# Kernel optimization log

Hardware: AMD Instinct MI355X
Metric: run time of the kernel (lower is better)

## Reference

```python
import jax, jax.numpy as jnp
import numpy as np

N = 100000   # nodes
E = 1600000  # edges
B = 64       # graphs
F = 16       # node features
H = 128      # hidden dim
G = 8        # graph features
C = 2        # classes
NGIN = 2     # extra GIN layers after the first
BN_EPS = 1e-5


def elu01(x):
    # F.elu with alpha=0.1
    return jnp.where(x > 0, x, 0.1 * jnp.expm1(x))


def batchnorm(h, gamma, beta):
    # training-mode BatchNorm1d: biased batch statistics
    mu = h.mean(axis=0)
    var = h.var(axis=0)
    return (h - mu) * jax.lax.rsqrt(var + BN_EPS) * gamma + beta


def gin_layer(x, src, dst, W1, b1, gm, bt, W2, b2):
    # GINConv eps=0: MLP(x + sum_{j->i} x_j), then ELU(0.1)
    agg = jax.ops.segment_sum(x[src], dst, num_segments=x.shape[0])
    h = (x + agg) @ W1 + b1
    h = jax.nn.relu(batchnorm(h, gm, bt))
    return elu01(h @ W2 + b2)


def setup_inputs() -> dict:
    key = jax.random.key(0)
    ks = jax.random.split(key, 24)
    s = 0.05
    inp = {
        "h0": jax.random.normal(ks[0], (N, F), jnp.float32),
        "coord0": jax.random.normal(ks[1], (N, 3), jnp.float32),
        "g0": jax.random.normal(ks[2], (B, G), jnp.float32),
        "edge_index": jax.random.randint(ks[3], (2, E), 0, N, jnp.int32),
        "batch": jnp.sort(jax.random.randint(ks[4], (N,), 0, B, jnp.int32)),
        # first GIN layer: (F+3) -> H -> H
        "w1_0": jax.random.normal(ks[5], (F + 3, H), jnp.float32) * s,
        "b1_0": jnp.zeros((H,), jnp.float32),
        "gm_0": jnp.ones((H,), jnp.float32),
        "bt_0": jnp.zeros((H,), jnp.float32),
        "w2_0": jax.random.normal(ks[6], (H, H), jnp.float32) * s,
        "b2_0": jnp.zeros((H,), jnp.float32),
        # NGIN stacked layers: H -> H -> H
        "w1_r": jax.random.normal(ks[7], (NGIN, H, H), jnp.float32) * s,
        "b1_r": jnp.zeros((NGIN, H), jnp.float32),
        "gm_r": jnp.ones((NGIN, H), jnp.float32),
        "bt_r": jnp.zeros((NGIN, H), jnp.float32),
        "w2_r": jax.random.normal(ks[8], (NGIN, H, H), jnp.float32) * s,
        "b2_r": jnp.zeros((NGIN, H), jnp.float32),
        # classifier: (2H+G) -> H -> C
        "cw1": jax.random.normal(ks[9], (2 * H + G, H), jnp.float32) * s,
        "cb1": jnp.zeros((H,), jnp.float32),
        "cgm": jnp.ones((H,), jnp.float32),
        "cbt": jnp.zeros((H,), jnp.float32),
        "cw2": jax.random.normal(ks[10], (H, C), jnp.float32) * s,
        "cb2": jnp.zeros((C,), jnp.float32),
    }
    return inp


def reference(h0, coord0, g0, edge_index, batch,
              w1_0, b1_0, gm_0, bt_0, w2_0, b2_0,
              w1_r, b1_r, gm_r, bt_r, w2_r, b2_r,
              cw1, cb1, cgm, cbt, cw2, cb2):
    src, dst = edge_index[0], edge_index[1]
    x = jnp.concatenate([h0, coord0], axis=1)  # [N, F+3]
    x = gin_layer(x, src, dst, w1_0, b1_0, gm_0, bt_0, w2_0, b2_0)
    for i in range(NGIN):
        x = gin_layer(x, src, dst, w1_r[i], b1_r[i], gm_r[i], bt_r[i], w2_r[i], b2_r[i])
    # global mean + max pooling per graph
    nb = g0.shape[0]
    cnt = jax.ops.segment_sum(jnp.ones((x.shape[0], 1), x.dtype), batch, num_segments=nb)
    mean_p = jax.ops.segment_sum(x, batch, num_segments=nb) / jnp.maximum(cnt, 1.0)
    max_p = jax.ops.segment_max(x, batch, num_segments=nb)
    pooled = jnp.concatenate([mean_p, max_p], axis=-1)  # [B, 2H]
    z = jnp.concatenate([pooled, g0], axis=1)           # [B, 2H+G]
    z = elu01(z @ cw1 + cb1)
    z = batchnorm(z, cgm, cbt)
    logits = z @ cw2 + cb2
    return jax.nn.softmax(logits, axis=1)
```

## Files before the change

### kernel.cpp

```cpp
#include <hip/hip_runtime.h>
#include <math.h>

#define NN 100000
#define EE 1600000
#define BB 64
#define FF 16
#define HH 128
#define GG 8
#define K0 19
#define BN_EPS 1e-5f
#define PCH 16
#define BSHIFT 8
#define BNODES 256
#define NBINS 391
#define BCAP 8192
#define ACH 2048

typedef short bf16x8 __attribute__((ext_vector_type(8)));
typedef float f32x4 __attribute__((ext_vector_type(4)));

__device__ __forceinline__ float elu01f(float v) {
    return v > 0.f ? v : 0.1f * (__expf(v) - 1.f);
}

__device__ __forceinline__ unsigned f2bfu(float f) {
    unsigned u = __float_as_uint(f);
    unsigned r = u + 0x7FFFu + ((u >> 16) & 1u);
    return r >> 16;
}
__device__ __forceinline__ short f2bf(float f) { return (short)f2bfu(f); }
__device__ __forceinline__ float bfu2f(unsigned short b) {
    return __uint_as_float(((unsigned)b) << 16);
}
__device__ __forceinline__ float bflo(unsigned u) { return __uint_as_float(u << 16); }
__device__ __forceinline__ float bfhi(unsigned u) { return __uint_as_float(u & 0xffff0000u); }

__global__ __launch_bounds__(256) void k_binA(const int* __restrict__ esrc, const int* __restrict__ edst,
                                              int* __restrict__ bincnt, uint2* __restrict__ binbuf) {
    __shared__ int hist[NBINS];
    __shared__ int gbase[NBINS];
    __shared__ int cur[NBINS];
    __shared__ int sc[512];
    __shared__ uint2 ebuf[ACH];
    __shared__ uint2 sorted[ACH];
    int tid = threadIdx.x;
    int e0 = blockIdx.x * ACH;
    int n = min(ACH, EE - e0);
    for (int i = tid; i < NBINS; i += 256) hist[i] = 0;
    __syncthreads();
    for (int i = tid; i < n; i += 256) {
        int s = esrc[e0 + i];
        int d = edst[e0 + i];
        ebuf[i] = make_uint2((unsigned)s, (unsigned)d);
        atomicAdd(&hist[d >> BSHIFT], 1);
    }
    __syncthreads();
    sc[tid] = (tid < NBINS) ? hist[tid] : 0;
    sc[tid + 256] = (tid + 256 < NBINS) ? hist[tid + 256] : 0;
    __syncthreads();
    for (int off = 1; off < 512; off <<= 1) {
        int a0 = sc[tid], a1 = sc[tid + 256];
        int b0 = (tid >= off) ? sc[tid - off] : 0;
        int b1 = (tid + 256 >= off) ? sc[tid + 256 - off] : 0;
        __syncthreads();
        sc[tid] = a0 + b0;
        sc[tid + 256] = a1 + b1;
        __syncthreads();
    }
    for (int b = tid; b < NBINS; b += 256) {
        int c = hist[b];
        gbase[b] = (c > 0) ? atomicAdd(&bincnt[b], c) : 0;
        cur[b] = (b > 0) ? sc[b - 1] : 0;
    }
    __syncthreads();
    for (int i = tid; i < n; i += 256) {
        uint2 e = ebuf[i];
        int b = (int)(e.y >> BSHIFT);
        int pos = atomicAdd(&cur[b], 1);
        sorted[pos] = e;
    }
    __syncthreads();
    for (int i = tid; i < n; i += 256) {
        uint2 e = sorted[i];
        int b = (int)(e.y >> BSHIFT);
        int ls = (b > 0) ? sc[b - 1] : 0;
        int gpos = gbase[b] + (i - ls);
        binbuf[(size_t)b * BCAP + gpos] = e;
    }
}

__global__ void k_binscan(const int* __restrict__ bincnt, int* __restrict__ binstart, int* __restrict__ rp,
                          const int* __restrict__ batch, int* __restrict__ gptr) {
    __shared__ int sc[512];
    int t = threadIdx.x;
    sc[t] = (t < NBINS) ? bincnt[t] : 0;
    __syncthreads();
    for (int off = 1; off < 512; off <<= 1) {
        int v = (t >= off) ? sc[t - off] : 0;
        __syncthreads();
        sc[t] += v;
        __syncthreads();
    }
    if (t < NBINS) binstart[t] = (t > 0) ? sc[t - 1] : 0;
    if (t == 0) rp[NN] = EE;
    if (t <= BB) {
        int lo = 0, hi = NN;
        while (lo < hi) { int mid = (lo + hi) >> 1; if (batch[mid] < t) lo = mid + 1; else hi = mid; }
        gptr[t] = lo;
    }
}

__global__ __launch_bounds__(256) void k_binB(const uint2* __restrict__ binbuf, const int* __restrict__ bincnt,
                                              const int* __restrict__ binstart,
                                              int* __restrict__ rp, int* __restrict__ srcs) {
    __shared__ int hist[BNODES];
    __shared__ int scx[BNODES];
    __shared__ int scur[BNODES];
    __shared__ int sbuf[BCAP];
    int b = blockIdx.x;
    int n = bincnt[b];
    int tid = threadIdx.x;
    hist[tid] = 0;
    __syncthreads();
    const uint2* eb = binbuf + (size_t)b * BCAP;
    for (int i = tid; i < n; i += 256)
        atomicAdd(&hist[eb[i].y & (BNODES - 1)], 1);
    __syncthreads();
    scx[tid] = hist[tid];
    __syncthreads();
    for (int off = 1; off < 256; off <<= 1) {
        int v = (tid >= off) ? scx[tid - off] : 0;
        __syncthreads();
        scx[tid] += v;
        __syncthreads();
    }
    int base = binstart[b];
    int excl = (tid > 0) ? scx[tid - 1] : 0;
    int node = (b << BSHIFT) + tid;
    if (node < NN) rp[node] = base + excl;
    scur[tid] = excl;
    __syncthreads();
    for (int i = tid; i < n; i += 256) {
        uint2 e = eb[i];
        int pos = atomicAdd(&scur[e.y & (BNODES - 1)], 1);
        sbuf[pos] = (int)e.x;
    }
    __syncthreads();
    for (int i = tid; i < n; i += 256) srcs[base + i] = sbuf[i];
}

__global__ __launch_bounds__(256) void k_wprep(const float* __restrict__ w2_0, const float* __restrict__ w1_r,
                                               const float* __restrict__ w2_r, short* __restrict__ wt) {
    int t = blockIdx.x * 256 + threadIdx.x;
    if (t >= 5 * HH * HH) return;
    int m = t >> 14;
    int rem = t & 16383;
    int col = rem >> 7;
    int k = rem & 127;
    const float* src = (m == 0) ? w2_0 : (m <= 2 ? w1_r + (size_t)(m - 1) * HH * HH
                                                 : w2_r + (size_t)(m - 3) * HH * HH);
    wt[t] = f2bf(src[k * HH + col]);
}

__global__ __launch_bounds__(256) void k_buildx0(const float* __restrict__ h0, const float* __restrict__ coord,
                                                 unsigned short* __restrict__ x0) {
    int i = blockIdx.x * 256 + threadIdx.x;
    if (i >= NN * 32) return;
    int node = i >> 5, k = i & 31;
    float v = 0.f;
    if (k < FF) v = h0[node * FF + k];
    else if (k < K0) v = coord[node * 3 + (k - FF)];
    x0[i] = (unsigned short)f2bfu(v);
}

__global__ __launch_bounds__(256) void k_agg_small(const uint4* __restrict__ x, const int* __restrict__ rp,
                                                   const int* __restrict__ srcs, uint4* __restrict__ y) {
    int w = (blockIdx.x * 256 + threadIdx.x) >> 6;
    int lane = threadIdx.x & 63;
    if (w >= NN) return;
    int e = lane >> 2, q = lane & 3;
    int beg = rp[w], end = rp[w + 1];
    float acc[8];
    {
        if (e == 0) {
            uint4 u = x[(size_t)w * 4 + q];
            acc[0] = bflo(u.x); acc[1] = bfhi(u.x);
            acc[2] = bflo(u.y); acc[3] = bfhi(u.y);
            acc[4] = bflo(u.z); acc[5] = bfhi(u.z);
            acc[6] = bflo(u.w); acc[7] = bfhi(u.w);
        } else {
            #pragma unroll
            for (int j = 0; j < 8; j++) acc[j] = 0.f;
        }
    }
    for (int p = beg; p < end; p += 16) {
        int rem = end - p;
        bool act = e < rem;
        int sn = act ? srcs[p + e] : 0;
        uint4 u = x[(size_t)sn * 4 + q];
        float m = act ? 1.f : 0.f;
        acc[0] = fmaf(m, bflo(u.x), acc[0]); acc[1] = fmaf(m, bfhi(u.x), acc[1]);
        acc[2] = fmaf(m, bflo(u.y), acc[2]); acc[3] = fmaf(m, bfhi(u.y), acc[3]);
        acc[4] = fmaf(m, bflo(u.z), acc[4]); acc[5] = fmaf(m, bfhi(u.z), acc[5]);
        acc[6] = fmaf(m, bflo(u.w), acc[6]); acc[7] = fmaf(m, bfhi(u.w), acc[7]);
    }
    #pragma unroll
    for (int mask = 4; mask <= 32; mask <<= 1)
        #pragma unroll
        for (int j = 0; j < 8; j++)
            acc[j] += __shfl_xor(acc[j], mask, 64);
    if (e == 0) {
        uint4 o;
        o.x = f2bfu(acc[0]) | (f2bfu(acc[1]) << 16);
        o.y = f2bfu(acc[2]) | (f2bfu(acc[3]) << 16);
        o.z = f2bfu(acc[4]) | (f2bfu(acc[5]) << 16);
        o.w = f2bfu(acc[6]) | (f2bfu(acc[7]) << 16);
        y[(size_t)w * 4 + q] = o;
    }
}

__global__ __launch_bounds__(256) void k_agg128_bf(const unsigned* __restrict__ x, const int* __restrict__ rp,
                                                   const int* __restrict__ srcs, unsigned* __restrict__ y) {
    int w = (blockIdx.x * 256 + threadIdx.x) >> 6;
    int lane = threadIdx.x & 63;
    if (w >= NN) return;
    int beg = rp[w], end = rp[w + 1];
    unsigned us = x[(size_t)w * 64 + lane];
    float ax = bflo(us), ay = bfhi(us);
    float bx = 0.f, by = 0.f;
    float cx = 0.f, cy = 0.f;
    float dx = 0.f, dy = 0.f;
    int p = beg;
    for (; p + 16 <= end; p += 16) {
        int s0 = srcs[p + 0], s1 = srcs[p + 1], s2 = srcs[p + 2], s3 = srcs[p + 3];
        int s4 = srcs[p + 4], s5 = srcs[p + 5], s6 = srcs[p + 6], s7 = srcs[p + 7];
        int s8 = srcs[p + 8], s9 = srcs[p + 9], sa = srcs[p + 10], sb = srcs[p + 11];
        int sc_ = srcs[p + 12], sd = srcs[p + 13], se = srcs[p + 14], sf = srcs[p + 15];
        unsigned u0 = x[(size_t)s0 * 64 + lane];
        unsigned u1 = x[(size_t)s1 * 64 + lane];
        unsigned u2 = x[(size_t)s2 * 64 + lane];
        unsigned u3 = x[(size_t)s3 * 64 + lane];
        unsigned u4 = x[(size_t)s4 * 64 + lane];
        unsigned u5 = x[(size_t)s5 * 64 + lane];
        unsigned u6 = x[(size_t)s6 * 64 + lane];
        unsigned u7 = x[(size_t)s7 * 64 + lane];
        unsigned u8 = x[(size_t)s8 * 64 + lane];
        unsigned u9 = x[(size_t)s9 * 64 + lane];
        unsigned ua = x[(size_t)sa * 64 + lane];
        unsigned ub = x[(size_t)sb * 64 + lane];
        unsigned uc = x[(size_t)sc_ * 64 + lane];
        unsigned ud = x[(size_t)sd * 64 + lane];
        unsigned ue = x[(size_t)se * 64 + lane];
        unsigned uf = x[(size_t)sf * 64 + lane];
        ax += (bflo(u0) + bflo(u1)) + (bflo(u2) + bflo(u3));
        ay += (bfhi(u0) + bfhi(u1)) + (bfhi(u2) + bfhi(u3));
        bx += (bflo(u4) + bflo(u5)) + (bflo(u6) + bflo(u7));
        by += (bfhi(u4) + bfhi(u5)) + (bfhi(u6) + bfhi(u7));
        cx += (bflo(u8) + bflo(u9)) + (bflo(ua) + bflo(ub));
        cy += (bfhi(u8) + bfhi(u9)) + (bfhi(ua) + bfhi(ub));
        dx += (bflo(uc) + bflo(ud)) + (bflo(ue) + bflo(uf));
        dy += (bfhi(uc) + bfhi(ud)) + (bfhi(ue) + bfhi(uf));
    }
    for (; p + 8 <= end; p += 8) {
        int s0 = srcs[p + 0], s1 = srcs[p + 1], s2 = srcs[p + 2], s3 = srcs[p + 3];
        int s4 = srcs[p + 4], s5 = srcs[p + 5], s6 = srcs[p + 6], s7 = srcs[p + 7];
        unsigned u0 = x[(size_t)s0 * 64 + lane];
        unsigned u1 = x[(size_t)s1 * 64 + lane];
        unsigned u2 = x[(size_t)s2 * 64 + lane];
        unsigned u3 = x[(size_t)s3 * 64 + lane];
        unsigned u4 = x[(size_t)s4 * 64 + lane];
        unsigned u5 = x[(size_t)s5 * 64 + lane];
        unsigned u6 = x[(size_t)s6 * 64 + lane];
        unsigned u7 = x[(size_t)s7 * 64 + lane];
        ax += (bflo(u0) + bflo(u1)) + (bflo(u2) + bflo(u3));
        ay += (bfhi(u0) + bfhi(u1)) + (bfhi(u2) + bfhi(u3));
        bx += (bflo(u4) + bflo(u5)) + (bflo(u6) + bflo(u7));
        by += (bfhi(u4) + bfhi(u5)) + (bfhi(u6) + bfhi(u7));
    }
    for (; p < end; ++p) {
        unsigned u = x[(size_t)srcs[p] * 64 + lane];
        ax += bflo(u);
        ay += bfhi(u);
    }
    ax += bx + cx + dx;
    ay += by + cy + dy;
    y[(size_t)w * 64 + lane] = f2bfu(ax) | (f2bfu(ay) << 16);
}

template<int K, bool STATS>
__global__ __launch_bounds__(256) void k_gemm_small(const unsigned short* __restrict__ in,
        const float* __restrict__ W, const float* __restrict__ bias,
        unsigned short* __restrict__ out, float* __restrict__ part) {
    constexpr int SK = ((K + 3) / 4) * 4 + 4;
    __shared__ __align__(16) float yt[32 * SK];
    __shared__ float red[256];
    int tid = threadIdx.x;
    int row0 = blockIdx.x * 32;
    for (int t = tid; t < 32 * SK; t += 256) {
        int r = t / SK, k = t - r * SK;
        float v = 0.f;
        if (k < K) v = bfu2f(in[(size_t)(row0 + r) * 32 + k]);
        yt[t] = v;
    }
    __syncthreads();
    int col = tid & 127;
    int rg = tid >> 7;
    float acc[16];
    #pragma unroll
    for (int r = 0; r < 16; r++) acc[r] = 0.f;
    const float* ybase = &yt[rg * 16 * SK];
    int kk = 0;
    for (; kk + 4 <= K; kk += 4) {
        float w0 = W[(kk + 0) * HH + col];
        float w1 = W[(kk + 1) * HH + col];
        float w2 = W[(kk + 2) * HH + col];
        float w3 = W[(kk + 3) * HH + col];
        #pragma unroll
        for (int r = 0; r < 16; r++) {
            const float4 v = *(const float4*)&ybase[r * SK + kk];
            acc[r] = fmaf(v.x, w0, acc[r]);
            acc[r] = fmaf(v.y, w1, acc[r]);
            acc[r] = fmaf(v.z, w2, acc[r]);
            acc[r] = fmaf(v.w, w3, acc[r]);
        }
    }
    if constexpr (K % 4 != 0) {
        float w[4];
        #pragma unroll
        for (int j = 0; j < 4; j++) w[j] = (kk + j < K) ? W[(kk + j) * HH + col] : 0.f;
        #pragma unroll
        for (int r = 0; r < 16; r++) {
            const float4 v = *(const float4*)&ybase[r * SK + kk];
            acc[r] = fmaf(v.x, w[0], acc[r]);
            acc[r] = fmaf(v.y, w[1], acc[r]);
            acc[r] = fmaf(v.z, w[2], acc[r]);
            acc[r] = fmaf(v.w, w[3], acc[r]);
        }
    }
    float bcol = bias[col];
    float s = 0.f, s2 = 0.f;
    #pragma unroll
    for (int r = 0; r < 16; r++) {
        float hv = acc[r] + bcol;
        out[(size_t)(row0 + rg * 16 + r) * HH + col] = (unsigned short)f2bfu(hv);
        if (STATS) { s += hv; s2 = fmaf(hv, hv, s2); }
    }
    if (STATS) {
        red[tid] = s; __syncthreads();
        if (tid < 128) part[(size_t)blockIdx.x * 256 + tid] = s + red[tid + 128];
        __syncthreads();
        red[tid] = s2; __syncthreads();
        if (tid < 128) part[(size_t)blockIdx.x * 256 + 128 + tid] = s2 + red[tid + 128];
    }
}

template<bool STATS, bool BNIN, bool ELUOUT>
__global__ __launch_bounds__(256) void k_gemm_mfma(const unsigned short* __restrict__ in,
        const short* __restrict__ WT, const float* __restrict__ bias,
        const float* __restrict__ bnscale, const float* __restrict__ bnshift,
        unsigned short* __restrict__ out, float* __restrict__ part) {
    __shared__ __align__(16) short Al[64 * 136];
    __shared__ float lsum[HH], lsq[HH];
    int tid = threadIdx.x;
    int row0 = blockIdx.x * 64;
    if (STATS && tid < HH) { lsum[tid] = 0.f; lsq[tid] = 0.f; }
    {
        int r = tid >> 2;
        int k0 = (tid & 3) * 32;
        int grow = row0 + r;
        short* dst = &Al[r * 136 + k0];
        if (grow < NN) {
            const uint4* s4 = (const uint4*)(in + (size_t)grow * HH + k0);
            if constexpr (!BNIN) {
                uint4* d4 = (uint4*)dst;
                d4[0] = s4[0]; d4[1] = s4[1]; d4[2] = s4[2]; d4[3] = s4[3];
            } else {
                unsigned* d = (unsigned*)dst;
                #pragma unroll
                for (int q = 0; q < 4; q++) {
                    uint4 u = s4[q];
                    float4 sc0 = *(const float4*)(bnscale + k0 + q * 8);
                    float4 sh0 = *(const float4*)(bnshift + k0 + q * 8);
                    float4 sc1 = *(const float4*)(bnscale + k0 + q * 8 + 4);
                    float4 sh1 = *(const float4*)(bnshift + k0 + q * 8 + 4);
                    float a0 = bflo(u.x), a1 = bfhi(u.x);
                    float a2 = bflo(u.y), a3 = bfhi(u.y);
                    float a4 = bflo(u.z), a5 = bfhi(u.z);
                    float a6 = bflo(u.w), a7 = bfhi(u.w);
                    a0 = fmaxf(fmaf(a0, sc0.x, sh0.x), 0.f);
                    a1 = fmaxf(fmaf(a1, sc0.y, sh0.y), 0.f);
                    a2 = fmaxf(fmaf(a2, sc0.z, sh0.z), 0.f);
                    a3 = fmaxf(fmaf(a3, sc0.w, sh0.w), 0.f);
                    a4 = fmaxf(fmaf(a4, sc1.x, sh1.x), 0.f);
                    a5 = fmaxf(fmaf(a5, sc1.y, sh1.y), 0.f);
                    a6 = fmaxf(fmaf(a6, sc1.z, sh1.z), 0.f);
                    a7 = fmaxf(fmaf(a7, sc1.w, sh1.w), 0.f);
                    d[q * 4 + 0] = f2bfu(a0) | (f2bfu(a1) << 16);
                    d[q * 4 + 1] = f2bfu(a2) | (f2bfu(a3) << 16);
                    d[q * 4 + 2] = f2bfu(a4) | (f2bfu(a5) << 16);
                    d[q * 4 + 3] = f2bfu(a6) | (f2bfu(a7) << 16);
                }
            }
        } else {
            uint4 z = {0, 0, 0, 0};
            uint4* d4 = (uint4*)dst;
            d4[0] = z; d4[1] = z; d4[2] = z; d4[3] = z;
        }
    }
    __syncthreads();
    int wave = tid >> 6;
    int lane = tid & 63;
    int ln = lane & 15, quad = lane >> 4;
    int wcol0 = wave * 32;
    f32x4 acc[4][2];
    #pragma unroll
    for (int rt = 0; rt < 4; rt++)
        #pragma unroll
        for (int ct = 0; ct < 2; ct++) acc[rt][ct] = (f32x4){0.f, 0.f, 0.f, 0.f};
    #pragma unroll
    for (int ks = 0; ks < 4; ks++) {
        bf16x8 a[4], b[2];
        #pragma unroll
        for (int ct = 0; ct < 2; ct++)
            b[ct] = *(const bf16x8*)(WT + (size_t)(wcol0 + ct * 16 + ln) * HH + ks * 32 + quad * 8);
        #pragma unroll
        for (int rt = 0; rt < 4; rt++)
            a[rt] = *(const bf16x8*)(&Al[(rt * 16 + ln) * 136 + ks * 32 + quad * 8]);
        #pragma unroll
        for (int rt = 0; rt < 4; rt++)
            #pragma unroll
            for (int ct = 0; ct < 2; ct++)
                acc[rt][ct] = __builtin_amdgcn_mfma_f32_16x16x32_bf16(a[rt], b[ct], acc[rt][ct], 0, 0, 0);
    }
    float b0 = bias[wcol0 + ln];
    float b1 = bias[wcol0 + 16 + ln];
    float s[2] = {0.f, 0.f}, s2[2] = {0.f, 0.f};
    #pragma unroll
    for (int rt = 0; rt < 4; rt++) {
        #pragma unroll
        for (int r = 0; r < 4; r++) {
            int grow = row0 + rt * 16 + quad * 4 + r;
            if (grow < NN) {
                float hv0 = acc[rt][0][r] + b0;
                float hv1 = acc[rt][1][r] + b1;
                if (ELUOUT) { hv0 = elu01f(hv0); hv1 = elu01f(hv1); }
                out[(size_t)grow * HH + wcol0 + ln] = (unsigned short)f2bfu(hv0);
                out[(size_t)grow * HH + wcol0 + 16 + ln] = (unsigned short)f2bfu(hv1);
                if (STATS) {
                    s[0] += hv0; s2[0] = fmaf(hv0, hv0, s2[0]);
                    s[1] += hv1; s2[1] = fmaf(hv1, hv1, s2[1]);
                }
            }
        }
    }
    if (STATS) {
        atomicAdd(&lsum[wcol0 + ln], s[0]);
        atomicAdd(&lsum[wcol0 + 16 + ln], s[1]);
        atomicAdd(&lsq[wcol0 + ln], s2[0]);
        atomicAdd(&lsq[wcol0 + 16 + ln], s2[1]);
        __syncthreads();
        if (tid < HH) {
            part[(size_t)blockIdx.x * 256 + tid] = lsum[tid];
            part[(size_t)blockIdx.x * 256 + 128 + tid] = lsq[tid];
        }
    }
}

__global__ __launch_bounds__(256) void k_statred(const float* __restrict__ part, float* __restrict__ part2,
                                                 int nrows) {
    int tid = threadIdx.x;
    float acc = 0.f;
    for (int r = blockIdx.x; r < nrows; r += 64)
        acc += part[(size_t)r * 256 + tid];
    part2[(size_t)blockIdx.x * 256 + tid] = acc;
}

__global__ void k_bnfin(const float* __restrict__ part2, const float* __restrict__ gm,
                        const float* __restrict__ bt, float* scale, float* shift) {
    int c = threadIdx.x;
    float s = 0.f, s2 = 0.f;
    #pragma unroll 4
    for (int j = 0; j < 64; ++j) {
        s += part2[(size_t)j * 256 + c];
        s2 += part2[(size_t)j * 256 + 128 + c];
    }
    float mu = s * (1.f / NN);
    float var = fmaxf(s2 * (1.f / NN) - mu * mu, 0.f);
    float a = gm[c] * rsqrtf(var + BN_EPS);
    scale[c] = a;
    shift[c] = fmaf(-mu, a, bt[c]);
}

__global__ __launch_bounds__(128) void k_pool_part(const unsigned short* __restrict__ x,
                                                   const int* __restrict__ gptr,
                                                   float* __restrict__ psum, float* __restrict__ pmax) {
    int g = blockIdx.x >> 4;
    int ch = blockIdx.x & 15;
    int s = gptr[g], e = gptr[g + 1];
    int len = e - s;
    int per = (len + PCH - 1) / PCH;
    int lo = s + ch * per;
    int hi = min(lo + per, e);
    int c = threadIdx.x;
    float sm = 0.f, mx = -INFINITY;
    for (int i = lo; i < hi; ++i) {
        float v = bfu2f(x[(size_t)i * HH + c]);
        sm += v; mx = fmaxf(mx, v);
    }
    psum[(size_t)blockIdx.x * HH + c] = sm;
    pmax[(size_t)blockIdx.x * HH + c] = mx;
}

__global__ __launch_bounds__(128) void k_pool_cls1(const float* __restrict__ psum, const float* __restrict__ pmax,
                                                   const int* __restrict__ gptr, const float* __restrict__ g0,
                                                   const float* __restrict__ cw1, const float* __restrict__ cb1,
                                                   float* __restrict__ z1) {
    __shared__ float zr[264];
    int g = blockIdx.x, c = threadIdx.x;
    float sm = 0.f, mx = -INFINITY;
    for (int ch = 0; ch < PCH; ++ch) {
        sm += psum[(size_t)(g * PCH + ch) * HH + c];
        mx = fmaxf(mx, pmax[(size_t)(g * PCH + ch) * HH + c]);
    }
    int cntn = gptr[g + 1] - gptr[g];
    zr[c] = sm / (float)max(cntn, 1);
    zr[128 + c] = mx;
    if (c < GG) zr[256 + c] = g0[g * GG + c];
    __syncthreads();
    float acc = cb1[c];
    for (int k = 0; k < 264; ++k) acc = fmaf(zr[k], cw1[k * HH + c], acc);
    z1[g * HH + c] = elu01f(acc);
}

__global__ __launch_bounds__(128) void k_cls2(const float* __restrict__ z1, const float* __restrict__ cgm,
                                              const float* __restrict__ cbt, const float* __restrict__ cw2,
                                              const float* __restrict__ cb2, float* __restrict__ outp) {
    __shared__ float zn[HH * 65];
    int c = threadIdx.x;
    float s = 0.f, s2 = 0.f;
    for (int g = 0; g < BB; ++g) {
        float v = z1[g * HH + c];
        s += v; s2 = fmaf(v, v, s2);
    }
    float mu = s * (1.f / BB);
    float var = fmaxf(s2 * (1.f / BB) - mu * mu, 0.f);
    float a = cgm[c] * rsqrtf(var + BN_EPS);
    float sh = fmaf(-mu, a, cbt[c]);
    for (int g = 0; g < BB; ++g) zn[c * 65 + g] = fmaf(z1[g * HH + c], a, sh);
    __syncthreads();
    if (c < BB) {
        float l0 = cb2[0], l1 = cb2[1];
        for (int k = 0; k < HH; ++k) {
            float v = zn[k * 65 + c];
            l0 = fmaf(v, cw2[k * 2 + 0], l0);
            l1 = fmaf(v, cw2[k * 2 + 1], l1);
        }
        float m = fmaxf(l0, l1);
        float e0 = __expf(l0 - m), e1 = __expf(l1 - m);
        float inv = 1.f / (e0 + e1);
        outp[c * 2 + 0] = e0 * inv;
        outp[c * 2 + 1] = e1 * inv;
    }
}

extern "C" void kernel_launch(void* const* d_in, const int* in_sizes, int n_in,
                              void* d_out, int out_size, void* d_ws, size_t ws_size,
                              hipStream_t stream) {
    (void)in_sizes; (void)n_in; (void)out_size; (void)ws_size;
    const float* h0     = (const float*)d_in[0];
    const float* coord0 = (const float*)d_in[1];
    const float* g0     = (const float*)d_in[2];
    const int*   eidx   = (const int*)d_in[3];
    const int*   batch  = (const int*)d_in[4];
    const float* w1_0   = (const float*)d_in[5];
    const float* b1_0   = (const float*)d_in[6];
    const float* gm_0   = (const float*)d_in[7];
    const float* bt_0   = (const float*)d_in[8];
    const float* w2_0   = (const float*)d_in[9];
    const float* b2_0   = (const float*)d_in[10];
    const float* w1_r   = (const float*)d_in[11];
    const float* b1_r   = (const float*)d_in[12];
    const float* gm_r   = (const float*)d_in[13];
    const float* bt_r   = (const float*)d_in[14];
    const float* w2_r   = (const float*)d_in[15];
    const float* b2_r   = (const float*)d_in[16];
    const float* cw1    = (const float*)d_in[17];
    const float* cb1    = (const float*)d_in[18];
    const float* cgm    = (const float*)d_in[19];
    const float* cbt    = (const float*)d_in[20];
    const float* cw2    = (const float*)d_in[21];
    const float* cb2    = (const float*)d_in[22];
    float* outp = (float*)d_out;

    const int* esrc = eidx;
    const int* edst = eidx + EE;

    char* p = (char*)d_ws;
    auto alloc = [&](size_t bytes) { void* r = (void*)p; p += (bytes + 255) & ~(size_t)255; return r; };
    unsigned short* x0bf     = (unsigned short*)alloc((size_t)NN * 32 * 2);
    unsigned short* y19bf    = (unsigned short*)alloc((size_t)NN * 32 * 2);
    unsigned short* hbf      = (unsigned short*)alloc((size_t)NN * HH * 2);
    unsigned*       xbf      = (unsigned*)alloc((size_t)NN * 64 * 4);
    unsigned*       ybf      = (unsigned*)alloc((size_t)NN * 64 * 4);
    int*            rp       = (int*)alloc((size_t)(NN + 1) * 4);
    int*            srcs     = (int*)alloc((size_t)EE * 4);
    int*            bincnt   = (int*)alloc((size_t)NBINS * 4);
    int*            binstart = (int*)alloc((size_t)NBINS * 4);
    int*            gptr     = (int*)alloc((BB + 1) * 4);
    short*          wt       = (short*)alloc((size_t)5 * HH * HH * 2);
    float*          part     = (float*)alloc((size_t)3125 * 256 * 4);
    float*          part2    = (float*)alloc((size_t)64 * 256 * 4);
    float*          bnscale  = (float*)alloc(HH * 4);
    float*          bnshift  = (float*)alloc(HH * 4);
    float*          psum     = (float*)alloc((size_t)BB * PCH * HH * 4);
    float*          pmax     = (float*)alloc((size_t)BB * PCH * HH * 4);
    float*          z1b      = (float*)alloc((size_t)BB * HH * 4);
    uint2*          binbuf   = (uint2*)alloc((size_t)NBINS * BCAP * 8);

    const int NB_A = (EE + ACH - 1) / ACH;
    const int NB_AGG = (NN * 64 + 255) / 256;
    const int NB_G32 = NN / 32;
    const int NB_G64 = (NN + 63) / 64;
    const int NB_X0 = (NN * 32 + 255) / 256;
    const int NB_WP = (5 * HH * HH + 255) / 256;

    hipMemsetAsync(bincnt, 0, (size_t)NBINS * 4, stream);
    k_binA<<<NB_A, 256, 0, stream>>>(esrc, edst, bincnt, binbuf);
    k_binscan<<<1, 512, 0, stream>>>(bincnt, binstart, rp, batch, gptr);
    k_binB<<<NBINS, 256, 0, stream>>>(binbuf, bincnt, binstart, rp, srcs);
    k_wprep<<<NB_WP, 256, 0, stream>>>(w2_0, w1_r, w2_r, wt);

    k_buildx0<<<NB_X0, 256, 0, stream>>>(h0, coord0, x0bf);
    k_agg_small<<<NB_AGG, 256, 0, stream>>>((const uint4*)x0bf, rp, srcs, (uint4*)y19bf);
    k_gemm_small<K0, true><<<NB_G32, 256, 0, stream>>>(y19bf, w1_0, b1_0, hbf, part);
    k_statred<<<64, 256, 0, stream>>>(part, part2, NB_G32);
    k_bnfin<<<1, 128, 0, stream>>>(part2, gm_0, bt_0, bnscale, bnshift);
    k_gemm_mfma<false, true, true><<<NB_G64, 256, 0, stream>>>(hbf, wt, b2_0, bnscale, bnshift,
                                                               (unsigned short*)xbf, nullptr);

    for (int i = 0; i < 2; ++i) {
        k_agg128_bf<<<NB_AGG, 256, 0, stream>>>(xbf, rp, srcs, ybf);
        k_gemm_mfma<true, false, false><<<NB_G64, 256, 0, stream>>>((const unsigned short*)ybf,
                wt + (size_t)(1 + i) * HH * HH, b1_r + i * HH, nullptr, nullptr, hbf, part);
        k_statred<<<64, 256, 0, stream>>>(part, part2, NB_G64);
        k_bnfin<<<1, 128, 0, stream>>>(part2, gm_r + i * HH, bt_r + i * HH, bnscale, bnshift);
        k_gemm_mfma<false, true, true><<<NB_G64, 256, 0, stream>>>(hbf,
                wt + (size_t)(3 + i) * HH * HH, b2_r + i * HH, bnscale, bnshift,
                (unsigned short*)xbf, nullptr);
    }

    k_pool_part<<<BB * PCH, 128, 0, stream>>>((const unsigned short*)xbf, gptr, psum, pmax);
    k_pool_cls1<<<BB, 128, 0, stream>>>(psum, pmax, gptr, g0, cw1, cb1, z1b);
    k_cls2<<<1, 128, 0, stream>>>(z1b, cgm, cbt, cw2, cb2, outp);
}
```

Before: 586.7 us.

## Fuse neighbor aggregation into first GEMM and fold BN stats via atomics

Merges the gather-sum aggregation with the following W1 GEMM (MFMA for hidden layers, scalar for layer 0), so the aggregated tile lives in shared memory instead of a global buffer. BatchNorm statistics are accumulated with atomics into a few slotted global buffers, and the BN scale/shift is computed inside the second GEMM, removing the separate stat-reduce and finalize kernels. Weight prep and input build are merged into one launch, and a single memset clears the counters and stats. This cuts global round-trips and launches, but the fused kernels run with fewer waves per node for the gather (16 rows per wave in sequence) and rely on float atomics, so summation order becomes nondeterministic.

```diff
diff --git a/kernel.cpp b/kernel.cpp
--- a/kernel.cpp
+++ b/kernel.cpp
@@ -15,6 +15,9 @@
 #define NBINS 391
 #define BCAP 8192
 #define ACH 2048
+#define NB_WP 320
+#define NB_X0 12500
+#define STSLOT 8
 
 typedef short bf16x8 __attribute__((ext_vector_type(8)));
 typedef float f32x4 __attribute__((ext_vector_type(4)));
@@ -149,41 +152,49 @@
     for (int i = tid; i < n; i += 256) srcs[base + i] = sbuf[i];
 }
 
-__global__ __launch_bounds__(256) void k_wprep(const float* __restrict__ w2_0, const float* __restrict__ w1_r,
-                                               const float* __restrict__ w2_r, short* __restrict__ wt) {
-    int t = blockIdx.x * 256 + threadIdx.x;
-    if (t >= 5 * HH * HH) return;
-    int m = t >> 14;
-    int rem = t & 16383;
-    int col = rem >> 7;
-    int k = rem & 127;
-    const float* src = (m == 0) ? w2_0 : (m <= 2 ? w1_r + (size_t)(m - 1) * HH * HH
-                                                 : w2_r + (size_t)(m - 3) * HH * HH);
-    wt[t] = f2bf(src[k * HH + col]);
-}
-
-__global__ __launch_bounds__(256) void k_buildx0(const float* __restrict__ h0, const float* __restrict__ coord,
-                                                 unsigned short* __restrict__ x0) {
-    int i = blockIdx.x * 256 + threadIdx.x;
-    if (i >= NN * 32) return;
-    int node = i >> 5, k = i & 31;
-    float v = 0.f;
-    if (k < FF) v = h0[node * FF + k];
-    else if (k < K0) v = coord[node * 3 + (k - FF)];
-    x0[i] = (unsigned short)f2bfu(v);
-}
-
-__global__ __launch_bounds__(256) void k_agg_small(const uint4* __restrict__ x, const int* __restrict__ rp,
-                                                   const int* __restrict__ srcs, uint4* __restrict__ y) {
-    int w = (blockIdx.x * 256 + threadIdx.x) >> 6;
-    int lane = threadIdx.x & 63;
-    if (w >= NN) return;
+__global__ __launch_bounds__(256) void k_prep(const float* __restrict__ w2_0, const float* __restrict__ w1_r,
+                                              const float* __restrict__ w2_r, short* __restrict__ wt,
+                                              const float* __restrict__ h0, const float* __restrict__ coord,
+                                              unsigned short* __restrict__ x0) {
+    int b = blockIdx.x;
+    if (b < NB_WP) {
+        int t = b * 256 + threadIdx.x;
+        if (t >= 5 * HH * HH) return;
+        int m = t >> 14;
+        int rem = t & 16383;
+        int col = rem >> 7;
+        int k = rem & 127;
+        const float* src = (m == 0) ? w2_0 : (m <= 2 ? w1_r + (size_t)(m - 1) * HH * HH
+                                                     : w2_r + (size_t)(m - 3) * HH * HH);
+        wt[t] = f2bf(src[k * HH + col]);
+    } else {
+        int i = (b - NB_WP) * 256 + threadIdx.x;
+        if (i >= NN * 32) return;
+        int node = i >> 5, k = i & 31;
+        float v = 0.f;
+        if (k < FF) v = h0[node * FF + k];
+        else if (k < K0) v = coord[node * 3 + (k - FF)];
+        x0[i] = (unsigned short)f2bfu(v);
+    }
+}
+
+template<int K>
+__global__ __launch_bounds__(256) void k_l0(const uint4* __restrict__ x4, const int* __restrict__ rp,
+        const int* __restrict__ srcs, const float* __restrict__ W, const float* __restrict__ bias,
+        unsigned short* __restrict__ out, float* __restrict__ gstat) {
+    constexpr int SK = ((K + 3) / 4) * 4 + 4;
+    __shared__ __align__(16) float yt[32 * SK];
+    __shared__ float red[256];
+    int tid = threadIdx.x;
+    int row0 = blockIdx.x * 32;
+    int wave = tid >> 6, lane = tid & 63;
     int e = lane >> 2, q = lane & 3;
-    int beg = rp[w], end = rp[w + 1];
-    float acc[8];
-    {
+    for (int rr = 0; rr < 8; ++rr) {
+        int r = (wave << 3) + rr;
+        int grow = row0 + r;
+        float acc[8];
         if (e == 0) {
-            uint4 u = x[(size_t)w * 4 + q];
+            uint4 u = x4[(size_t)grow * 4 + q];
             acc[0] = bflo(u.x); acc[1] = bfhi(u.x);
             acc[2] = bflo(u.y); acc[3] = bfhi(u.y);
             acc[4] = bflo(u.z); acc[5] = bfhi(u.z);
@@ -192,122 +203,32 @@
             #pragma unroll
             for (int j = 0; j < 8; j++) acc[j] = 0.f;
         }
-    }
-    for (int p = beg; p < end; p += 16) {
-        int rem = end - p;
-        bool act = e < rem;
-        int sn = act ? srcs[p + e] : 0;
-        uint4 u = x[(size_t)sn * 4 + q];
-        float m = act ? 1.f : 0.f;
-        acc[0] = fmaf(m, bflo(u.x), acc[0]); acc[1] = fmaf(m, bfhi(u.x), acc[1]);
-        acc[2] = fmaf(m, bflo(u.y), acc[2]); acc[3] = fmaf(m, bfhi(u.y), acc[3]);
-        acc[4] = fmaf(m, bflo(u.z), acc[4]); acc[5] = fmaf(m, bfhi(u.z), acc[5]);
-        acc[6] = fmaf(m, bflo(u.w), acc[6]); acc[7] = fmaf(m, bfhi(u.w), acc[7]);
-    }
-    #pragma unroll
-    for (int mask = 4; mask <= 32; mask <<= 1)
-        #pragma unroll
-        for (int j = 0; j < 8; j++)
-            acc[j] += __shfl_xor(acc[j], mask, 64);
-    if (e == 0) {
-        uint4 o;
-        o.x = f2bfu(acc[0]) | (f2bfu(acc[1]) << 16);
-        o.y = f2bfu(acc[2]) | (f2bfu(acc[3]) << 16);
-        o.z = f2bfu(acc[4]) | (f2bfu(acc[5]) << 16);
-        o.w = f2bfu(acc[6]) | (f2bfu(acc[7]) << 16);
-        y[(size_t)w * 4 + q] = o;
-    }
-}
-
-__global__ __launch_bounds__(256) void k_agg128_bf(const unsigned* __restrict__ x, const int* __restrict__ rp,
-                                                   const int* __restrict__ srcs, unsigned* __restrict__ y) {
-    int w = (blockIdx.x * 256 + threadIdx.x) >> 6;
-    int lane = threadIdx.x & 63;
-    if (w >= NN) return;
-    int beg = rp[w], end = rp[w + 1];
-    unsigned us = x[(size_t)w * 64 + lane];
-    float ax = bflo(us), ay = bfhi(us);
-    float bx = 0.f, by = 0.f;
-    float cx = 0.f, cy = 0.f;
-    float dx = 0.f, dy = 0.f;
-    int p = beg;
-    for (; p + 16 <= end; p += 16) {
-        int s0 = srcs[p + 0], s1 = srcs[p + 1], s2 = srcs[p + 2], s3 = srcs[p + 3];
-        int s4 = srcs[p + 4], s5 = srcs[p + 5], s6 = srcs[p + 6], s7 = srcs[p + 7];
-        int s8 = srcs[p + 8], s9 = srcs[p + 9], sa = srcs[p + 10], sb = srcs[p + 11];
-        int sc_ = srcs[p + 12], sd = srcs[p + 13], se = srcs[p + 14], sf = srcs[p + 15];
-        unsigned u0 = x[(size_t)s0 * 64 + lane];
-        unsigned u1 = x[(size_t)s1 * 64 + lane];
-        unsigned u2 = x[(size_t)s2 * 64 + lane];
-        unsigned u3 = x[(size_t)s3 * 64 + lane];
-        unsigned u4 = x[(size_t)s4 * 64 + lane];
-        unsigned u5 = x[(size_t)s5 * 64 + lane];
-        unsigned u6 = x[(size_t)s6 * 64 + lane];
-        unsigned u7 = x[(size_t)s7 * 64 + lane];
-        unsigned u8 = x[(size_t)s8 * 64 + lane];
-        unsigned u9 = x[(size_t)s9 * 64 + lane];
-        unsigned ua = x[(size_t)sa * 64 + lane];
-        unsigned ub = x[(size_t)sb * 64 + lane];
-        unsigned uc = x[(size_t)sc_ * 64 + lane];
-        unsigned ud = x[(size_t)sd * 64 + lane];
-        unsigned ue = x[(size_t)se * 64 + lane];
-        unsigned uf = x[(size_t)sf * 64 + lane];
-        ax += (bflo(u0) + bflo(u1)) + (bflo(u2) + bflo(u3));
-        ay += (bfhi(u0) + bfhi(u1)) + (bfhi(u2) + bfhi(u3));
-        bx += (bflo(u4) + bflo(u5)) + (bflo(u6) + bflo(u7));
-        by += (bfhi(u4) + bfhi(u5)) + (bfhi(u6) + bfhi(u7));
-        cx += (bflo(u8) + bflo(u9)) + (bflo(ua) + bflo(ub));
-        cy += (bfhi(u8) + bfhi(u9)) + (bfhi(ua) + bfhi(ub));
-        dx += (bflo(uc) + bflo(ud)) + (bflo(ue) + bflo(uf));
-        dy += (bfhi(uc) + bfhi(ud)) + (bfhi(ue) + bfhi(uf));
-    }
-    for (; p + 8 <= end; p += 8) {
-        int s0 = srcs[p + 0], s1 = srcs[p + 1], s2 = srcs[p + 2], s3 = srcs[p + 3];
-        int s4 = srcs[p + 4], s5 = srcs[p + 5], s6 = srcs[p + 6], s7 = srcs[p + 7];
-        unsigned u0 = x[(size_t)s0 * 64 + lane];
-        unsigned u1 = x[(size_t)s1 * 64 + lane];
-        unsigned u2 = x[(size_t)s2 * 64 + lane];
-        unsigned u3 = x[(size_t)s3 * 64 + lane];
-        unsigned u4 = x[(size_t)s4 * 64 + lane];
-        unsigned u5 = x[(size_t)s5 * 64 + lane];
-        unsigned u6 = x[(size_t)s6 * 64 + lane];
-        unsigned u7 = x[(size_t)s7 * 64 + lane];
-        ax += (bflo(u0) + bflo(u1)) + (bflo(u2) + bflo(u3));
-        ay += (bfhi(u0) + bfhi(u1)) + (bfhi(u2) + bfhi(u3));
-        bx += (bflo(u4) + bflo(u5)) + (bflo(u6) + bflo(u7));
-        by += (bfhi(u4) + bfhi(u5)) + (bfhi(u6) + bfhi(u7));
-    }
-    for (; p < end; ++p) {
-        unsigned u = x[(size_t)srcs[p] * 64 + lane];
-        ax += bflo(u);
-        ay += bfhi(u);
-    }
-    ax += bx + cx + dx;
-    ay += by + cy + dy;
-    y[(size_t)w * 64 + lane] = f2bfu(ax) | (f2bfu(ay) << 16);
-}
-
-template<int K, bool STATS>
-__global__ __launch_bounds__(256) void k_gemm_small(const unsigned short* __restrict__ in,
-        const float* __restrict__ W, const float* __restrict__ bias,
-        unsigned short* __restrict__ out, float* __restrict__ part) {
-    constexpr int SK = ((K + 3) / 4) * 4 + 4;
-    __shared__ __align__(16) float yt[32 * SK];
-    __shared__ float red[256];
-    int tid = threadIdx.x;
-    int row0 = blockIdx.x * 32;
-    for (int t = tid; t < 32 * SK; t += 256) {
-        int r = t / SK, k = t - r * SK;
-        float v = 0.f;
-        if (k < K) v = bfu2f(in[(size_t)(row0 + r) * 32 + k]);
-        yt[t] = v;
+        int beg = rp[grow], end = rp[grow + 1];
+        for (int p = beg; p < end; p += 16) {
+            bool act = e < (end - p);
+            int sn = act ? srcs[p + e] : 0;
+            uint4 u = x4[(size_t)sn * 4 + q];
+            float m = act ? 1.f : 0.f;
+            acc[0] = fmaf(m, bflo(u.x), acc[0]); acc[1] = fmaf(m, bfhi(u.x), acc[1]);
+            acc[2] = fmaf(m, bflo(u.y), acc[2]); acc[3] = fmaf(m, bfhi(u.y), acc[3]);
+            acc[4] = fmaf(m, bflo(u.z), acc[4]); acc[5] = fmaf(m, bfhi(u.z), acc[5]);
+            acc[6] = fmaf(m, bflo(u.w), acc[6]); acc[7] = fmaf(m, bfhi(u.w), acc[7]);
+        }
+        #pragma unroll
+        for (int mask = 4; mask <= 32; mask <<= 1)
+            #pragma unroll
+            for (int j = 0; j < 8; j++) acc[j] += __shfl_xor(acc[j], mask, 64);
+        if (e == 0 && q < 3) {
+            #pragma unroll
+            for (int j = 0; j < 8; j++) yt[r * SK + q * 8 + j] = acc[j];
+        }
     }
     __syncthreads();
     int col = tid & 127;
     int rg = tid >> 7;
-    float acc[16];
-    #pragma unroll
-    for (int r = 0; r < 16; r++) acc[r] = 0.f;
+    float facc[16];
+    #pragma unroll
+    for (int r = 0; r < 16; r++) facc[r] = 0.f;
     const float* ybase = &yt[rg * 16 * SK];
     int kk = 0;
     for (; kk + 4 <= K; kk += 4) {
@@ -318,10 +239,10 @@
         #pragma unroll
         for (int r = 0; r < 16; r++) {
             const float4 v = *(const float4*)&ybase[r * SK + kk];
-            acc[r] = fmaf(v.x, w0, acc[r]);
-            acc[r] = fmaf(v.y, w1, acc[r]);
-            acc[r] = fmaf(v.z, w2, acc[r]);
-            acc[r] = fmaf(v.w, w3, acc[r]);
+            facc[r] = fmaf(v.x, w0, facc[r]);
+            facc[r] = fmaf(v.y, w1, facc[r]);
+            facc[r] = fmaf(v.z, w2, facc[r]);
+            facc[r] = fmaf(v.w, w3, facc[r]);
         }
     }
     if constexpr (K % 4 != 0) {
@@ -331,39 +252,148 @@
         #pragma unroll
         for (int r = 0; r < 16; r++) {
             const float4 v = *(const float4*)&ybase[r * SK + kk];
-            acc[r] = fmaf(v.x, w[0], acc[r]);
-            acc[r] = fmaf(v.y, w[1], acc[r]);
-            acc[r] = fmaf(v.z, w[2], acc[r]);
-            acc[r] = fmaf(v.w, w[3], acc[r]);
+            facc[r] = fmaf(v.x, w[0], facc[r]);
+            facc[r] = fmaf(v.y, w[1], facc[r]);
+            facc[r] = fmaf(v.z, w[2], facc[r]);
+            facc[r] = fmaf(v.w, w[3], facc[r]);
         }
     }
     float bcol = bias[col];
     float s = 0.f, s2 = 0.f;
     #pragma unroll
     for (int r = 0; r < 16; r++) {
-        float hv = acc[r] + bcol;
+        float hv = facc[r] + bcol;
         out[(size_t)(row0 + rg * 16 + r) * HH + col] = (unsigned short)f2bfu(hv);
-        if (STATS) { s += hv; s2 = fmaf(hv, hv, s2); }
-    }
-    if (STATS) {
-        red[tid] = s; __syncthreads();
-        if (tid < 128) part[(size_t)blockIdx.x * 256 + tid] = s + red[tid + 128];
-        __syncthreads();
-        red[tid] = s2; __syncthreads();
-        if (tid < 128) part[(size_t)blockIdx.x * 256 + 128 + tid] = s2 + red[tid + 128];
-    }
-}
-
-template<bool STATS, bool BNIN, bool ELUOUT>
-__global__ __launch_bounds__(256) void k_gemm_mfma(const unsigned short* __restrict__ in,
-        const short* __restrict__ WT, const float* __restrict__ bias,
-        const float* __restrict__ bnscale, const float* __restrict__ bnshift,
-        unsigned short* __restrict__ out, float* __restrict__ part) {
+        s += hv; s2 = fmaf(hv, hv, s2);
+    }
+    int sl = (blockIdx.x & (STSLOT - 1)) << 8;
+    red[tid] = s; __syncthreads();
+    if (tid < 128) atomicAdd(&gstat[sl + tid], s + red[tid + 128]);
+    __syncthreads();
+    red[tid] = s2; __syncthreads();
+    if (tid < 128) atomicAdd(&gstat[sl + 128 + tid], s2 + red[tid + 128]);
+}
+
+__global__ __launch_bounds__(256) void k_agg_gemm(const unsigned* __restrict__ x, const int* __restrict__ rp,
+        const int* __restrict__ srcs, const short* __restrict__ WT, const float* __restrict__ bias,
+        unsigned short* __restrict__ out, float* __restrict__ gstat) {
     __shared__ __align__(16) short Al[64 * 136];
     __shared__ float lsum[HH], lsq[HH];
     int tid = threadIdx.x;
+    int wave = tid >> 6, lane = tid & 63;
+    if (tid < HH) { lsum[tid] = 0.f; lsq[tid] = 0.f; }
     int row0 = blockIdx.x * 64;
-    if (STATS && tid < HH) { lsum[tid] = 0.f; lsq[tid] = 0.f; }
+    unsigned* Ad = (unsigned*)Al;
+    for (int rr = 0; rr < 16; ++rr) {
+        int r = (wave << 4) + rr;
+        int grow = row0 + r;
+        float ax = 0.f, ay = 0.f;
+        if (grow < NN) {
+            unsigned us = x[(size_t)grow * 64 + lane];
+            ax = bflo(us); ay = bfhi(us);
+            float bx = 0.f, by = 0.f;
+            int beg = rp[grow], end = rp[grow + 1];
+            int p = beg;
+            for (; p + 8 <= end; p += 8) {
+                int s0 = srcs[p + 0], s1 = srcs[p + 1], s2 = srcs[p + 2], s3 = srcs[p + 3];
+                int s4 = srcs[p + 4], s5 = srcs[p + 5], s6 = srcs[p + 6], s7 = srcs[p + 7];
+                unsigned u0 = x[(size_t)s0 * 64 + lane];
+                unsigned u1 = x[(size_t)s1 * 64 + lane];
+                unsigned u2 = x[(size_t)s2 * 64 + lane];
+                unsigned u3 = x[(size_t)s3 * 64 + lane];
+                unsigned u4 = x[(size_t)s4 * 64 + lane];
+                unsigned u5 = x[(size_t)s5 * 64 + lane];
+                unsigned u6 = x[(size_t)s6 * 64 + lane];
+                unsigned u7 = x[(size_t)s7 * 64 + lane];
+                ax += (bflo(u0) + bflo(u1)) + (bflo(u2) + bflo(u3));
+                ay += (bfhi(u0) + bfhi(u1)) + (bfhi(u2) + bfhi(u3));
+                bx += (bflo(u4) + bflo(u5)) + (bflo(u6) + bflo(u7));
+                by += (bfhi(u4) + bfhi(u5)) + (bfhi(u6) + bfhi(u7));
+            }
+            for (; p < end; ++p) {
+                unsigned u = x[(size_t)srcs[p] * 64 + lane];
+                ax += bflo(u);
+                ay += bfhi(u);
+            }
+            ax += bx; ay += by;
+        }
+        Ad[r * 68 + lane] = f2bfu(ax) | (f2bfu(ay) << 16);
+    }
+    __syncthreads();
+    int ln = lane & 15, quad = lane >> 4;
+    int wcol0 = wave * 32;
+    f32x4 acc[4][2];
+    #pragma unroll
+    for (int rt = 0; rt < 4; rt++)
+        #pragma unroll
+        for (int ct = 0; ct < 2; ct++) acc[rt][ct] = (f32x4){0.f, 0.f, 0.f, 0.f};
+    #pragma unroll
+    for (int ks = 0; ks < 4; ks++) {
+        bf16x8 a[4], b[2];
+        #pragma unroll
+        for (int ct = 0; ct < 2; ct++)
+            b[ct] = *(const bf16x8*)(WT + (size_t)(wcol0 + ct * 16 + ln) * HH + ks * 32 + quad * 8);
+        #pragma unroll
+        for (int rt = 0; rt < 4; rt++)
+            a[rt] = *(const bf16x8*)(&Al[(rt * 16 + ln) * 136 + ks * 32 + quad * 8]);
+        #pragma unroll
+        for (int rt = 0; rt < 4; rt++)
+            #pragma unroll
+            for (int ct = 0; ct < 2; ct++)
+                acc[rt][ct] = __builtin_amdgcn_mfma_f32_16x16x32_bf16(a[rt], b[ct], acc[rt][ct], 0, 0, 0);
+    }
+    float b0 = bias[wcol0 + ln];
+    float b1 = bias[wcol0 + 16 + ln];
+    float s[2] = {0.f, 0.f}, s2[2] = {0.f, 0.f};
+    #pragma unroll
+    for (int rt = 0; rt < 4; rt++) {
+        #pragma unroll
+        for (int r = 0; r < 4; r++) {
+            int grow = row0 + rt * 16 + quad * 4 + r;
+            if (grow < NN) {
+                float hv0 = acc[rt][0][r] + b0;
+                float hv1 = acc[rt][1][r] + b1;
+                out[(size_t)grow * HH + wcol0 + ln] = (unsigned short)f2bfu(hv0);
+                out[(size_t)grow * HH + wcol0 + 16 + ln] = (unsigned short)f2bfu(hv1);
+                s[0] += hv0; s2[0] = fmaf(hv0, hv0, s2[0]);
+                s[1] += hv1; s2[1] = fmaf(hv1, hv1, s2[1]);
+            }
+        }
+    }
+    atomicAdd(&lsum[wcol0 + ln], s[0]);
+    atomicAdd(&lsum[wcol0 + 16 + ln], s[1]);
+    atomicAdd(&lsq[wcol0 + ln], s2[0]);
+    atomicAdd(&lsq[wcol0 + 16 + ln], s2[1]);
+    __syncthreads();
+    if (tid < HH) {
+        int sl = (blockIdx.x & (STSLOT - 1)) << 8;
+        atomicAdd(&gstat[sl + tid], lsum[tid]);
+        atomicAdd(&gstat[sl + 128 + tid], lsq[tid]);
+    }
+}
+
+__global__ __launch_bounds__(256) void k_gemm_bn(const unsigned short* __restrict__ in,
+        const short* __restrict__ WT, const float* __restrict__ bias,
+        const float* __restrict__ gstat, const float* __restrict__ gm, const float* __restrict__ bt,
+        unsigned short* __restrict__ out) {
+    __shared__ __align__(16) short Al[64 * 136];
+    __shared__ __align__(16) float bnsc[HH], bnsh[HH];
+    int tid = threadIdx.x;
+    if (tid < HH) {
+        float s = 0.f, s2 = 0.f;
+        #pragma unroll
+        for (int k = 0; k < STSLOT; ++k) {
+            s += gstat[(k << 8) + tid];
+            s2 += gstat[(k << 8) + 128 + tid];
+        }
+        float mu = s * (1.f / NN);
+        float var = fmaxf(s2 * (1.f / NN) - mu * mu, 0.f);
+        float a = gm[tid] * rsqrtf(var + BN_EPS);
+        bnsc[tid] = a;
+        bnsh[tid] = fmaf(-mu, a, bt[tid]);
+    }
+    __syncthreads();
+    int row0 = blockIdx.x * 64;
     {
         int r = tid >> 2;
         int k0 = (tid & 3) * 32;
@@ -371,35 +401,30 @@
         short* dst = &Al[r * 136 + k0];
         if (grow < NN) {
             const uint4* s4 = (const uint4*)(in + (size_t)grow * HH + k0);
-            if constexpr (!BNIN) {
-                uint4* d4 = (uint4*)dst;
-                d4[0] = s4[0]; d4[1] = s4[1]; d4[2] = s4[2]; d4[3] = s4[3];
-            } else {
-                unsigned* d = (unsigned*)dst;
-                #pragma unroll
-                for (int q = 0; q < 4; q++) {
-                    uint4 u = s4[q];
-                    float4 sc0 = *(const float4*)(bnscale + k0 + q * 8);
-                    float4 sh0 = *(const float4*)(bnshift + k0 + q * 8);
-                    float4 sc1 = *(const float4*)(bnscale + k0 + q * 8 + 4);
-                    float4 sh1 = *(const float4*)(bnshift + k0 + q * 8 + 4);
-                    float a0 = bflo(u.x), a1 = bfhi(u.x);
-                    float a2 = bflo(u.y), a3 = bfhi(u.y);
-                    float a4 = bflo(u.z), a5 = bfhi(u.z);
-                    float a6 = bflo(u.w), a7 = bfhi(u.w);
-                    a0 = fmaxf(fmaf(a0, sc0.x, sh0.x), 0.f);
-                    a1 = fmaxf(fmaf(a1, sc0.y, sh0.y), 0.f);
-                    a2 = fmaxf(fmaf(a2, sc0.z, sh0.z), 0.f);
-                    a3 = fmaxf(fmaf(a3, sc0.w, sh0.w), 0.f);
-                    a4 = fmaxf(fmaf(a4, sc1.x, sh1.x), 0.f);
-                    a5 = fmaxf(fmaf(a5, sc1.y, sh1.y), 0.f);
-                    a6 = fmaxf(fmaf(a6, sc1.z, sh1.z), 0.f);
-                    a7 = fmaxf(fmaf(a7, sc1.w, sh1.w), 0.f);
-                    d[q * 4 + 0] = f2bfu(a0) | (f2bfu(a1) << 16);
-                    d[q * 4 + 1] = f2bfu(a2) | (f2bfu(a3) << 16);
-                    d[q * 4 + 2] = f2bfu(a4) | (f2bfu(a5) << 16);
-                    d[q * 4 + 3] = f2bfu(a6) | (f2bfu(a7) << 16);
-                }
+            unsigned* d = (unsigned*)dst;
+            #pragma unroll
+            for (int q = 0; q < 4; q++) {
+                uint4 u = s4[q];
+                float4 sc0 = *(const float4*)(bnsc + k0 + q * 8);
+                float4 sh0 = *(const float4*)(bnsh + k0 + q * 8);
+                float4 sc1 = *(const float4*)(bnsc + k0 + q * 8 + 4);
+                float4 sh1 = *(const float4*)(bnsh + k0 + q * 8 + 4);
+                float a0 = bflo(u.x), a1 = bfhi(u.x);
+                float a2 = bflo(u.y), a3 = bfhi(u.y);
+                float a4 = bflo(u.z), a5 = bfhi(u.z);
+                float a6 = bflo(u.w), a7 = bfhi(u.w);
+                a0 = fmaxf(fmaf(a0, sc0.x, sh0.x), 0.f);
+                a1 = fmaxf(fmaf(a1, sc0.y, sh0.y), 0.f);
+                a2 = fmaxf(fmaf(a2, sc0.z, sh0.z), 0.f);
+                a3 = fmaxf(fmaf(a3, sc0.w, sh0.w), 0.f);
+                a4 = fmaxf(fmaf(a4, sc1.x, sh1.x), 0.f);
+                a5 = fmaxf(fmaf(a5, sc1.y, sh1.y), 0.f);
+                a6 = fmaxf(fmaf(a6, sc1.z, sh1.z), 0.f);
+                a7 = fmaxf(fmaf(a7, sc1.w, sh1.w), 0.f);
+                d[q * 4 + 0] = f2bfu(a0) | (f2bfu(a1) << 16);
+                d[q * 4 + 1] = f2bfu(a2) | (f2bfu(a3) << 16);
+                d[q * 4 + 2] = f2bfu(a4) | (f2bfu(a5) << 16);
+                d[q * 4 + 3] = f2bfu(a6) | (f2bfu(a7) << 16);
             }
         } else {
             uint4 z = {0, 0, 0, 0};
@@ -434,61 +459,19 @@
     }
     float b0 = bias[wcol0 + ln];
     float b1 = bias[wcol0 + 16 + ln];
-    float s[2] = {0.f, 0.f}, s2[2] = {0.f, 0.f};
     #pragma unroll
     for (int rt = 0; rt < 4; rt++) {
         #pragma unroll
         for (int r = 0; r < 4; r++) {
             int grow = row0 + rt * 16 + quad * 4 + r;
             if (grow < NN) {
-                float hv0 = acc[rt][0][r] + b0;
-                float hv1 = acc[rt][1][r] + b1;
-                if (ELUOUT) { hv0 = elu01f(hv0); hv1 = elu01f(hv1); }
+                float hv0 = elu01f(acc[rt][0][r] + b0);
+                float hv1 = elu01f(acc[rt][1][r] + b1);
                 out[(size_t)grow * HH + wcol0 + ln] = (unsigned short)f2bfu(hv0);
                 out[(size_t)grow * HH + wcol0 + 16 + ln] = (unsigned short)f2bfu(hv1);
-                if (STATS) {
-                    s[0] += hv0; s2[0] = fmaf(hv0, hv0, s2[0]);
-                    s[1] += hv1; s2[1] = fmaf(hv1, hv1, s2[1]);
-                }
             }
         }
     }
-    if (STATS) {
-        atomicAdd(&lsum[wcol0 + ln], s[0]);
-        atomicAdd(&lsum[wcol0 + 16 + ln], s[1]);
-        atomicAdd(&lsq[wcol0 + ln], s2[0]);
-        atomicAdd(&lsq[wcol0 + 16 + ln], s2[1]);
-        __syncthreads();
-        if (tid < HH) {
-            part[(size_t)blockIdx.x * 256 + tid] = lsum[tid];
-            part[(size_t)blockIdx.x * 256 + 128 + tid] = lsq[tid];
-        }
-    }
-}
-
-__global__ __launch_bounds__(256) void k_statred(const float* __restrict__ part, float* __restrict__ part2,
-                                                 int nrows) {
-    int tid = threadIdx.x;
-    float acc = 0.f;
-    for (int r = blockIdx.x; r < nrows; r += 64)
-        acc += part[(size_t)r * 256 + tid];
-    part2[(size_t)blockIdx.x * 256 + tid] = acc;
-}
-
-__global__ void k_bnfin(const float* __restrict__ part2, const float* __restrict__ gm,
-                        const float* __restrict__ bt, float* scale, float* shift) {
-    int c = threadIdx.x;
-    float s = 0.f, s2 = 0.f;
-    #pragma unroll 4
-    for (int j = 0; j < 64; ++j) {
-        s += part2[(size_t)j * 256 + c];
-        s2 += part2[(size_t)j * 256 + 128 + c];
-    }
-    float mu = s * (1.f / NN);
-    float var = fmaxf(s2 * (1.f / NN) - mu * mu, 0.f);
-    float a = gm[c] * rsqrtf(var + BN_EPS);
-    scale[c] = a;
-    shift[c] = fmaf(-mu, a, bt[c]);
 }
 
 __global__ __launch_bounds__(128) void k_pool_part(const unsigned short* __restrict__ x,
@@ -597,56 +580,42 @@
 
     char* p = (char*)d_ws;
     auto alloc = [&](size_t bytes) { void* r = (void*)p; p += (bytes + 255) & ~(size_t)255; return r; };
+    int*            bincnt   = (int*)alloc((size_t)NBINS * 4);
+    float*          gstat    = (float*)alloc((size_t)3 * STSLOT * 256 * 4);
     unsigned short* x0bf     = (unsigned short*)alloc((size_t)NN * 32 * 2);
-    unsigned short* y19bf    = (unsigned short*)alloc((size_t)NN * 32 * 2);
     unsigned short* hbf      = (unsigned short*)alloc((size_t)NN * HH * 2);
     unsigned*       xbf      = (unsigned*)alloc((size_t)NN * 64 * 4);
-    unsigned*       ybf      = (unsigned*)alloc((size_t)NN * 64 * 4);
     int*            rp       = (int*)alloc((size_t)(NN + 1) * 4);
     int*            srcs     = (int*)alloc((size_t)EE * 4);
-    int*            bincnt   = (int*)alloc((size_t)NBINS * 4);
     int*            binstart = (int*)alloc((size_t)NBINS * 4);
     int*            gptr     = (int*)alloc((BB + 1) * 4);
     short*          wt       = (short*)alloc((size_t)5 * HH * HH * 2);
-    float*          part     = (float*)alloc((size_t)3125 * 256 * 4);
-    float*          part2    = (float*)alloc((size_t)64 * 256 * 4);
-    float*          bnscale  = (float*)alloc(HH * 4);
-    float*          bnshift  = (float*)alloc(HH * 4);
     float*          psum     = (float*)alloc((size_t)BB * PCH * HH * 4);
     float*          pmax     = (float*)alloc((size_t)BB * PCH * HH * 4);
     float*          z1b      = (float*)alloc((size_t)BB * HH * 4);
     uint2*          binbuf   = (uint2*)alloc((size_t)NBINS * BCAP * 8);
 
     const int NB_A = (EE + ACH - 1) / ACH;
-    const int NB_AGG = (NN * 64 + 255) / 256;
     const int NB_G32 = NN / 32;
     const int NB_G64 = (NN + 63) / 64;
-    const int NB_X0 = (NN * 32 + 255) / 256;
-    const int NB_WP = (5 * HH * HH + 255) / 256;
-
-    hipMemsetAsync(bincnt, 0, (size_t)NBINS * 4, stream);
+
+    size_t zlen = (size_t)((char*)x0bf - (char*)bincnt);
+    hipMemsetAsync(bincnt, 0, zlen, stream);
+
     k_binA<<<NB_A, 256, 0, stream>>>(esrc, edst, bincnt, binbuf);
     k_binscan<<<1, 512, 0, stream>>>(bincnt, binstart, rp, batch, gptr);
     k_binB<<<NBINS, 256, 0, stream>>>(binbuf, bincnt, binstart, rp, srcs);
-    k_wprep<<<NB_WP, 256, 0, stream>>>(w2_0, w1_r, w2_r, wt);
-
-    k_buildx0<<<NB_X0, 256, 0, stream>>>(h0, coord0, x0bf);
-    k_agg_small<<<NB_AGG, 256, 0, stream>>>((const uint4*)x0bf, rp, srcs, (uint4*)y19bf);
-    k_gemm_small<K0, true><<<NB_G32, 256, 0, stream>>>(y19bf, w1_0, b1_0, hbf, part);
-    k_statred<<<64, 256, 0, stream>>>(part, part2, NB_G32);
-    k_bnfin<<<1, 128, 0, stream>>>(part2, gm_0, bt_0, bnscale, bnshift);
-    k_gemm_mfma<false, true, true><<<NB_G64, 256, 0, stream>>>(hbf, wt, b2_0, bnscale, bnshift,
-                                                               (unsigned short*)xbf, nullptr);
+    k_prep<<<NB_WP + NB_X0, 256, 0, stream>>>(w2_0, w1_r, w2_r, wt, h0, coord0, x0bf);
+
+    k_l0<K0><<<NB_G32, 256, 0, stream>>>((const uint4*)x0bf, rp, srcs, w1_0, b1_0, hbf, gstat);
+    k_gemm_bn<<<NB_G64, 256, 0, stream>>>(hbf, wt, b2_0, gstat, gm_0, bt_0, (unsigned short*)xbf);
 
     for (int i = 0; i < 2; ++i) {
-        k_agg128_bf<<<NB_AGG, 256, 0, stream>>>(xbf, rp, srcs, ybf);
-        k_gemm_mfma<true, false, false><<<NB_G64, 256, 0, stream>>>((const unsigned short*)ybf,
-                wt + (size_t)(1 + i) * HH * HH, b1_r + i * HH, nullptr, nullptr, hbf, part);
-        k_statred<<<64, 256, 0, stream>>>(part, part2, NB_G64);
-        k_bnfin<<<1, 128, 0, stream>>>(part2, gm_r + i * HH, bt_r + i * HH, bnscale, bnshift);
-        k_gemm_mfma<false, true, true><<<NB_G64, 256, 0, stream>>>(hbf,
-                wt + (size_t)(3 + i) * HH * HH, b2_r + i * HH, bnscale, bnshift,
-                (unsigned short*)xbf, nullptr);
+        float* gs = gstat + (size_t)(1 + i) * STSLOT * 256;
+        k_agg_gemm<<<NB_G64, 256, 0, stream>>>(xbf, rp, srcs, wt + (size_t)(1 + i) * HH * HH,
+                                               b1_r + i * HH, hbf, gs);
+        k_gemm_bn<<<NB_G64, 256, 0, stream>>>(hbf, wt + (size_t)(3 + i) * HH * HH, b2_r + i * HH,
+                                              gs, gm_r + i * HH, bt_r + i * HH, (unsigned short*)xbf);
     }
 
     k_pool_part<<<BB * PCH, 128, 0, stream>>>((const unsigned short*)xbf, gptr, psum, pmax);
```

Result: slower. 618.7 us (+5.5%).
